# Kernel optimization log

Measured on AMD Instinct MI355X. Metric: run time of the kernel, lower is better.

The kernel has to match this reference:

```python
import jax, jax.numpy as jnp
import numpy as np

CONTEXT = 3  # config['context']
B, H, W = 8, 256, 256
NBR = 2 * CONTEXT  # number of similarity branches


def _conv(x, w, b):
    # x: [N, Cin, H, W], w: [Cout, Cin, kh, kw], SAME padding, stride 1
    y = jax.lax.conv_general_dilated(x, w, (1, 1), 'SAME',
                                     dimension_numbers=('NCHW', 'OIHW', 'NCHW'))
    return y + b[None, :, None, None]


def setup_inputs() -> dict:
    key = jax.random.key(0)
    ks = jax.random.split(key, 5)
    x = jax.random.normal(ks[0], (B, 2 * CONTEXT + 1, H, W), dtype=jnp.float32)
    # kaiming-ish scaled inits
    W1 = jax.random.normal(ks[1], (NBR, 64, 2, 3, 3), dtype=jnp.float32) * (2.0 / (64 * 9)) ** 0.5
    b1 = jnp.zeros((NBR, 64), dtype=jnp.float32)
    W2 = jax.random.normal(ks[2], (NBR, 1, 64, 1, 1), dtype=jnp.float32) * (2.0 / 1) ** 0.5 * 0.1
    b2 = jnp.zeros((NBR, 1), dtype=jnp.float32)
    Wm = jax.random.normal(ks[3], (7, 7, 3, 3), dtype=jnp.float32) * (2.0 / (7 * 9)) ** 0.5
    bm = jnp.zeros((7,), dtype=jnp.float32)
    return {'x': x, 'W1': W1, 'b1': b1, 'W2': W2, 'b2': b2, 'Wm': Wm, 'bm': bm}


def reference(x, W1, b1, W2, b2, Wm, bm):
    # mode == 'context' path just returns x; this implements the main path.
    base = x[:, CONTEXT:CONTEXT + 1]                                  # [B,1,H,W]
    checks = jnp.concatenate([x[:, :CONTEXT], x[:, CONTEXT + 1:]], axis=1)  # [B,6,H,W]
    check_e = checks[:, :, None]                                      # [B,6,1,H,W]
    base_e = jnp.broadcast_to(base[:, None], check_e.shape)           # [B,6,1,H,W]
    # channel order: pre-frames -> (base, check); post-frames -> (check, base)
    ch0 = jnp.concatenate([base_e[:, :CONTEXT], check_e[:, CONTEXT:]], axis=2 - 2 + 2)  # placeholder
    ch0 = jnp.concatenate([base_e[:, :CONTEXT], check_e[:, CONTEXT:]], axis=1)
    ch1 = jnp.concatenate([check_e[:, :CONTEXT], base_e[:, CONTEXT:]], axis=1)
    pairs = jnp.concatenate([ch0, ch1], axis=2)                       # [B,6,2,H,W]
    pairs = jnp.swapaxes(pairs, 0, 1)                                 # [6,B,2,H,W]

    def branch(pair, w1, bb1, w2, bb2):
        h = jax.nn.relu(_conv(pair, w1, bb1))                         # [B,64,H,W]
        return jax.nn.sigmoid(_conv(h, w2, bb2))                      # [B,1,H,W]

    sims = jax.vmap(branch)(pairs, W1, b1, W2, b2)                    # [6,B,1,H,W]
    weighted = sims[:, :, 0] * jnp.swapaxes(checks, 0, 1)             # [6,B,H,W]
    weighted = jnp.swapaxes(weighted, 0, 1)                           # [B,6,H,W]
    combined = jnp.concatenate([weighted[:, :CONTEXT], base, weighted[:, CONTEXT:]], axis=1)  # [B,7,H,W]
    return _conv(combined, Wm, bm)                                    # [B,7,H,W]
```

## Files before the change

### kernel.cpp

```cpp
#include <hip/hip_runtime.h>
#include <math.h>

#define Bn 8
#define Hn 256
#define Wn 256
#define HW (Hn * Wn)
#define ROWS 4
#define RP 264
#define ZW (12 * RP)

typedef __attribute__((ext_vector_type(8))) short bf16x8;
typedef __attribute__((ext_vector_type(4))) float f32x4;

__device__ __forceinline__ unsigned int pk_bits(unsigned int lo,
                                                unsigned int hi) {
  return __builtin_amdgcn_perm(hi, lo, 0x07060302u);
}
__device__ __forceinline__ unsigned int pk_bf16(float lo, float hi) {
  return pk_bits(__float_as_uint(lo), __float_as_uint(hi));
}

__device__ __constant__ const int T0c[8] = {0, 1, 2, 9, 10, 11, 3, 4};
__device__ __constant__ const int T1c[8] = {6, 7, 8, 15, 16, 17, 12, 13};
__device__ __constant__ const int T2c[8] = {5, 14, -1, -1, -1, -1, -1, -1};

__global__ __launch_bounds__(256) void sim_kernel(
    const float* __restrict__ x,
    const float* __restrict__ W1,
    const float* __restrict__ b1,
    const float* __restrict__ W2,
    const float* __restrict__ b2,
    float* __restrict__ comb)
{
  __shared__ float rowsF[12 * RP + 64];
  __shared__ uint4 wq[4][64];

  int bi = blockIdx.x;
  int n  = bi >> 9;
  int b  = (bi >> 6) & 7;
  int h0 = (bi & 63) * ROWS;
  int cc = (n < 3) ? n : n + 1;
  int t = threadIdx.x;

  const float* xb     = x + (size_t)b * 7 * HW;
  const float* basep  = xb + 3 * HW;
  const float* checkp = xb + (size_t)cc * HW;

  {
    int f = t >> 6, qq = (t >> 4) & 3, m = t & 15;
    int bsrc = (n < 3) ? 0 : 1;
    const float* wch = W1 + ((size_t)(n * 64 + 16 * f + m)) * 18;
    unsigned int kv[4];
#pragma unroll
    for (int jj = 0; jj < 4; ++jj) {
      int ja = 2 * jj, jb = 2 * jj + 1;
      int ta = (qq == 0) ? T0c[ja] : (qq == 1) ? T1c[ja]
               : (qq == 2) ? T2c[ja] : -1;
      int tb = (qq == 0) ? T0c[jb] : (qq == 1) ? T1c[jb]
               : (qq == 2) ? T2c[jb] : -1;
      float va = 0.f, vb = 0.f;
      if (ta >= 0) {
        int pl = ta / 9, rem = ta - pl * 9;
        va = wch[(pl ? 1 - bsrc : bsrc) * 9 + rem];
      }
      if (tb >= 0) {
        int pl = tb / 9, rem = tb - pl * 9;
        vb = wch[(pl ? 1 - bsrc : bsrc) * 9 + rem];
      }
      kv[jj] = pk_bf16(va, vb);
    }
    wq[f][(qq << 4) + m] = make_uint4(kv[0], kv[1], kv[2], kv[3]);
  }

  int lane = t & 63, wvid = t >> 6;
  int q = lane >> 4, m_ = lane & 15;
  float w2v[4][4];
  f32x4 b1vv[4];
#pragma unroll
  for (int f = 0; f < 4; ++f) {
    float4 tw = *(const float4*)&W2[n * 64 + 16 * f + 4 * q];
    float4 tb = *(const float4*)&b1[n * 64 + 16 * f + 4 * q];
    w2v[f][0] = tw.x; w2v[f][1] = tw.y; w2v[f][2] = tw.z; w2v[f][3] = tw.w;
    b1vv[f][0] = tb.x; b1vv[f][1] = tb.y;
    b1vv[f][2] = tb.z; b1vv[f][3] = tb.w;
  }
  float bb = b2[n];

  {
    int col = (t & 63) << 2;
#pragma unroll
    for (int it = 0; it < 3; ++it) {
      int rf = it * 4 + (t >> 6);
      int pl = (rf >= 6) ? 1 : 0;
      int j  = rf - pl * 6;
      int hh = h0 - 1 + j;
      const float* src = pl ? checkp : basep;
      float4 val = make_float4(0.f, 0.f, 0.f, 0.f);
      if ((unsigned)hh < (unsigned)Hn)
        val = *(const float4*)(src + hh * Wn + col);
      *(float4*)&rowsF[rf * RP + 4 + col] = val;
    }
    if (t < 12) {
      rowsF[t * RP + 3] = 0.f;
      rowsF[t * RP + 260] = 0.f;
    }
    if (t >= 192) rowsF[ZW + (t - 192)] = 0.f;
  }

  const unsigned int* rowsU = (const unsigned int*)rowsF;
  unsigned int addr[8], vbit[8];
#pragma unroll
  for (int jh = 0; jh < 8; ++jh) {
    int tap = (q == 0) ? T0c[jh] : (q == 1) ? T1c[jh]
              : (q == 2) ? T2c[jh] : -1;
    if (tap >= 0) {
      int pl = tap / 9, rem = tap - pl * 9;
      int rr = rem / 3, dx = rem - rr * 3;
      addr[jh] = (pl * 6 + rr) * RP + 3 + dx + wvid * 64 + m_;
      vbit[jh] = 1u;
    } else {
      addr[jh] = (unsigned)ZW;
      vbit[jh] = 0u;
    }
  }

  __syncthreads();

  bf16x8 afrag[4];
#pragma unroll
  for (int f = 0; f < 4; ++f) afrag[f] = *(const bf16x8*)&wq[f][lane];

  float* combcc = comb + ((size_t)b * 7 + cc) * HW;
  float* comb3  = comb + ((size_t)b * 7 + 3) * HW;
  int pxs = wvid * 64 + lane;

#pragma unroll 2
  for (int r = 0; r < ROWS; ++r) {
    int h = h0 + r;
    unsigned int rowoff = (unsigned)(r * RP);

    unsigned int base[8];
#pragma unroll
    for (int jh = 0; jh < 8; ++jh) base[jh] = addr[jh] + vbit[jh] * rowoff;

    float g[4];
#pragma unroll
    for (int half = 0; half < 2; ++half) {
      unsigned int dlo[8], dhi[8];
#pragma unroll
      for (int jh = 0; jh < 8; ++jh) {
        dlo[jh] = rowsU[base[jh] + half * 32];
        dhi[jh] = rowsU[base[jh] + half * 32 + 16];
      }
#pragma unroll
      for (int j = 0; j < 2; ++j) {
        const unsigned int* d = j ? dhi : dlo;
        union { unsigned int u[4]; bf16x8 v; } bu;
#pragma unroll
        for (int jj = 0; jj < 4; ++jj)
          bu.u[jj] = pk_bits(d[2 * jj], d[2 * jj + 1]);

        f32x4 acc[4];
#pragma unroll
        for (int f = 0; f < 4; ++f)
          acc[f] = __builtin_amdgcn_mfma_f32_16x16x32_bf16(afrag[f], bu.v,
                                                           b1vv[f], 0, 0, 0);

        float spA = 0.f, spB = 0.f;
#pragma unroll
        for (int rr = 0; rr < 4; ++rr) {
          spA = fmaf(w2v[0][rr], fmaxf(acc[0][rr], 0.f), spA);
          spB = fmaf(w2v[2][rr], fmaxf(acc[2][rr], 0.f), spB);
          spA = fmaf(w2v[1][rr], fmaxf(acc[1][rr], 0.f), spA);
          spB = fmaf(w2v[3][rr], fmaxf(acc[3][rr], 0.f), spB);
        }
        float sp = spA + spB;
        sp += __shfl_xor(sp, 16, 64);
        sp += __shfl_xor(sp, 32, 64);
        sp += bb;

        float e = __builtin_amdgcn_exp2f(sp * -1.442695041f);
        g[2 * half + j] = __builtin_amdgcn_rcpf(1.f + e);
      }
    }

    int hi = lane >> 4;
    float gsel = (hi == 0) ? g[0] : (hi == 1) ? g[1] : (hi == 2) ? g[2] : g[3];
    float ccv = rowsF[(6 + r + 1) * RP + 4 + pxs];
    combcc[h * Wn + pxs] = gsel * ccv;
    if (n == 0) comb3[h * Wn + pxs] = rowsF[(r + 1) * RP + 4 + pxs];
  }
}

__global__ __launch_bounds__(256) void mix_kernel(
    const float* __restrict__ comb,
    const float* __restrict__ Wm,
    const float* __restrict__ bm,
    float* __restrict__ out)
{
  __shared__ float mr[28 * RP];

  int bi = blockIdx.x;
  int b  = bi >> 7;
  int h0 = (bi & 127) << 1;
  int t = threadIdx.x;

  for (int u = t; u < 28 * 64; u += 256) {
    int rf = u >> 6;
    int col = (u & 63) << 2;
    int ic = rf >> 2, j = rf & 3;
    int hh = h0 - 1 + j;
    float4 v = make_float4(0.f, 0.f, 0.f, 0.f);
    if ((unsigned)hh < (unsigned)Hn)
      v = *(const float4*)(comb + ((size_t)b * 7 + ic) * HW + hh * Wn + col);
    *(float4*)&mr[rf * RP + 4 + col] = v;
  }
  if (t < 28) {
    mr[t * RP + 3] = 0.f;
    mr[t * RP + 260] = 0.f;
  }
  __syncthreads();

  int r   = t >> 7;
  int px0 = (t & 127) << 1;
  int h   = h0 + r;

  float acc[7][2];
#pragma unroll
  for (int oc = 0; oc < 7; ++oc) {
    float bv = bm[oc];
    acc[oc][0] = bv;
    acc[oc][1] = bv;
  }

#pragma unroll 2
  for (int ic = 0; ic < 7; ++ic) {
    float w[3][4];
#pragma unroll
    for (int dy = 0; dy < 3; ++dy) {
      const float* rp = &mr[(ic * 4 + r + dy) * RP + 3 + px0];
      w[dy][0] = rp[0]; w[dy][1] = rp[1];
      w[dy][2] = rp[2]; w[dy][3] = rp[3];
    }
    const float* wp = Wm + ic * 9;
#pragma unroll
    for (int oc = 0; oc < 7; ++oc) {
      const float* wo = wp + oc * 63;
#pragma unroll
      for (int dy = 0; dy < 3; ++dy)
#pragma unroll
        for (int dx = 0; dx < 3; ++dx) {
          float wvv = wo[dy * 3 + dx];
          acc[oc][0] = fmaf(wvv, w[dy][0 + dx], acc[oc][0]);
          acc[oc][1] = fmaf(wvv, w[dy][1 + dx], acc[oc][1]);
        }
    }
  }

  float* ob = out + (size_t)b * 7 * HW + h * Wn + px0;
#pragma unroll
  for (int oc = 0; oc < 7; ++oc)
    *(float2*)(ob + (size_t)oc * HW) = make_float2(acc[oc][0], acc[oc][1]);
}

extern "C" void kernel_launch(void* const* d_in, const int* in_sizes, int n_in,
                              void* d_out, int out_size, void* d_ws, size_t ws_size,
                              hipStream_t stream) {
  const float* x  = (const float*)d_in[0];
  const float* W1 = (const float*)d_in[1];
  const float* b1 = (const float*)d_in[2];
  const float* W2 = (const float*)d_in[3];
  const float* b2 = (const float*)d_in[4];
  const float* Wm = (const float*)d_in[5];
  const float* bm = (const float*)d_in[6];
  float* out  = (float*)d_out;
  float* comb = (float*)d_ws;

  sim_kernel<<<6 * 8 * (Hn / ROWS), 256, 0, stream>>>(x, W1, b1, W2, b2, comb);
  mix_kernel<<<8 * (Hn / 2), 256, 0, stream>>>(comb, Wm, bm, out);
}
```

Baseline: 124.8 us.

## Split sim kernel into single-wave blocks per 64-column strip, drop LDS weight staging

Result: slower. 142.5 us (+14.2%).

```diff
diff --git a/kernel.cpp b/kernel.cpp
--- a/kernel.cpp
+++ b/kernel.cpp
@@ -6,8 +6,8 @@
 #define Wn 256
 #define HW (Hn * Wn)
 #define ROWS 4
-#define RP 264
-#define ZW (12 * RP)
+#define SRP 68
+#define SZW (12 * SRP)
 
 typedef __attribute__((ext_vector_type(8))) short bf16x8;
 typedef __attribute__((ext_vector_type(4))) float f32x4;
@@ -20,11 +20,7 @@
   return pk_bits(__float_as_uint(lo), __float_as_uint(hi));
 }
 
-__device__ __constant__ const int T0c[8] = {0, 1, 2, 9, 10, 11, 3, 4};
-__device__ __constant__ const int T1c[8] = {6, 7, 8, 15, 16, 17, 12, 13};
-__device__ __constant__ const int T2c[8] = {5, 14, -1, -1, -1, -1, -1, -1};
-
-__global__ __launch_bounds__(256) void sim_kernel(
+__global__ __launch_bounds__(64) void sim_kernel(
     const float* __restrict__ x,
     const float* __restrict__ W1,
     const float* __restrict__ b1,
@@ -32,48 +28,69 @@
     const float* __restrict__ b2,
     float* __restrict__ comb)
 {
-  __shared__ float rowsF[12 * RP + 64];
-  __shared__ uint4 wq[4][64];
+  __shared__ float rowsS[12 * SRP + 64];
 
   int bi = blockIdx.x;
-  int n  = bi >> 9;
-  int b  = (bi >> 6) & 7;
-  int h0 = (bi & 63) * ROWS;
+  int n  = bi >> 11;
+  int rem = bi & 2047;
+  int b  = rem >> 8;
+  int c  = (rem >> 2) & 63;
+  int s  = rem & 3;
+  int h0 = c * ROWS;
+  int w0 = s * 64;
   int cc = (n < 3) ? n : n + 1;
-  int t = threadIdx.x;
+
+  int lane = threadIdx.x;
+  int q = lane >> 4, m_ = lane & 15;
 
   const float* xb     = x + (size_t)b * 7 * HW;
   const float* basep  = xb + 3 * HW;
   const float* checkp = xb + (size_t)cc * HW;
 
-  {
-    int f = t >> 6, qq = (t >> 4) & 3, m = t & 15;
-    int bsrc = (n < 3) ? 0 : 1;
-    const float* wch = W1 + ((size_t)(n * 64 + 16 * f + m)) * 18;
+#pragma unroll
+  for (int rf = 0; rf < 12; ++rf) {
+    int pl = (rf >= 6) ? 1 : 0;
+    int j  = rf - pl * 6;
+    int hh = h0 - 1 + j;
+    const float* src = pl ? checkp : basep;
+    bool okh = (unsigned)hh < (unsigned)Hn;
+    int col = w0 - 1 + lane;
+    float v = (okh && (unsigned)col < (unsigned)Wn) ? src[hh * Wn + col] : 0.f;
+    rowsS[rf * SRP + lane] = v;
+    if (lane < 2) {
+      int col2 = w0 + 63 + lane;
+      float v2 = (okh && (unsigned)col2 < (unsigned)Wn)
+                     ? src[hh * Wn + col2] : 0.f;
+      rowsS[rf * SRP + 64 + lane] = v2;
+    }
+  }
+  rowsS[SZW + lane] = 0.f;
+
+  int bsrc = (n < 3) ? 0 : 1;
+  bf16x8 afrag[4];
+#pragma unroll
+  for (int f = 0; f < 4; ++f) {
+    const float* wch = W1 + ((size_t)(n * 64 + 16 * f + m_)) * 18;
     unsigned int kv[4];
 #pragma unroll
     for (int jj = 0; jj < 4; ++jj) {
-      int ja = 2 * jj, jb = 2 * jj + 1;
-      int ta = (qq == 0) ? T0c[ja] : (qq == 1) ? T1c[ja]
-               : (qq == 2) ? T2c[ja] : -1;
-      int tb = (qq == 0) ? T0c[jb] : (qq == 1) ? T1c[jb]
-               : (qq == 2) ? T2c[jb] : -1;
-      float va = 0.f, vb = 0.f;
-      if (ta >= 0) {
-        int pl = ta / 9, rem = ta - pl * 9;
-        va = wch[(pl ? 1 - bsrc : bsrc) * 9 + rem];
-      }
-      if (tb >= 0) {
-        int pl = tb / 9, rem = tb - pl * 9;
-        vb = wch[(pl ? 1 - bsrc : bsrc) * 9 + rem];
-      }
-      kv[jj] = pk_bf16(va, vb);
-    }
-    wq[f][(qq << 4) + m] = make_uint4(kv[0], kv[1], kv[2], kv[3]);
-  }
-
-  int lane = t & 63, wvid = t >> 6;
-  int q = lane >> 4, m_ = lane & 15;
+      int k0 = 8 * q + 2 * jj, k1 = k0 + 1;
+      float v0 = 0.f, v1 = 0.f;
+      if (k0 < 18) {
+        int pl = (k0 >= 9) ? 1 : 0;
+        v0 = wch[(pl ? 1 - bsrc : bsrc) * 9 + (k0 - 9 * pl)];
+      }
+      if (k1 < 18) {
+        int pl = (k1 >= 9) ? 1 : 0;
+        v1 = wch[(pl ? 1 - bsrc : bsrc) * 9 + (k1 - 9 * pl)];
+      }
+      kv[jj] = pk_bf16(v0, v1);
+    }
+    union { unsigned int u[4]; bf16x8 v; } au;
+    au.u[0] = kv[0]; au.u[1] = kv[1]; au.u[2] = kv[2]; au.u[3] = kv[3];
+    afrag[f] = au.v;
+  }
+
   float w2v[4][4];
   f32x4 b1vv[4];
 #pragma unroll
@@ -86,58 +103,30 @@
   }
   float bb = b2[n];
 
-  {
-    int col = (t & 63) << 2;
-#pragma unroll
-    for (int it = 0; it < 3; ++it) {
-      int rf = it * 4 + (t >> 6);
-      int pl = (rf >= 6) ? 1 : 0;
-      int j  = rf - pl * 6;
-      int hh = h0 - 1 + j;
-      const float* src = pl ? checkp : basep;
-      float4 val = make_float4(0.f, 0.f, 0.f, 0.f);
-      if ((unsigned)hh < (unsigned)Hn)
-        val = *(const float4*)(src + hh * Wn + col);
-      *(float4*)&rowsF[rf * RP + 4 + col] = val;
-    }
-    if (t < 12) {
-      rowsF[t * RP + 3] = 0.f;
-      rowsF[t * RP + 260] = 0.f;
-    }
-    if (t >= 192) rowsF[ZW + (t - 192)] = 0.f;
-  }
-
-  const unsigned int* rowsU = (const unsigned int*)rowsF;
+  const unsigned int* rowsU = (const unsigned int*)rowsS;
   unsigned int addr[8], vbit[8];
 #pragma unroll
   for (int jh = 0; jh < 8; ++jh) {
-    int tap = (q == 0) ? T0c[jh] : (q == 1) ? T1c[jh]
-              : (q == 2) ? T2c[jh] : -1;
-    if (tap >= 0) {
-      int pl = tap / 9, rem = tap - pl * 9;
-      int rr = rem / 3, dx = rem - rr * 3;
-      addr[jh] = (pl * 6 + rr) * RP + 3 + dx + wvid * 64 + m_;
+    int k = 8 * q + jh;
+    if (k < 18) {
+      int pl = (k >= 9) ? 1 : 0;
+      int rem2 = k - 9 * pl;
+      int rr = rem2 / 3, dx = rem2 - rr * 3;
+      addr[jh] = (pl * 6 + rr) * SRP + m_ + dx;
       vbit[jh] = 1u;
     } else {
-      addr[jh] = (unsigned)ZW;
+      addr[jh] = (unsigned)SZW;
       vbit[jh] = 0u;
     }
   }
-
-  __syncthreads();
-
-  bf16x8 afrag[4];
-#pragma unroll
-  for (int f = 0; f < 4; ++f) afrag[f] = *(const bf16x8*)&wq[f][lane];
 
   float* combcc = comb + ((size_t)b * 7 + cc) * HW;
   float* comb3  = comb + ((size_t)b * 7 + 3) * HW;
-  int pxs = wvid * 64 + lane;
 
 #pragma unroll 2
   for (int r = 0; r < ROWS; ++r) {
     int h = h0 + r;
-    unsigned int rowoff = (unsigned)(r * RP);
+    unsigned int rowoff = (unsigned)(r * SRP);
 
     unsigned int base[8];
 #pragma unroll
@@ -184,14 +173,15 @@
       }
     }
 
-    int hi = lane >> 4;
-    float gsel = (hi == 0) ? g[0] : (hi == 1) ? g[1] : (hi == 2) ? g[2] : g[3];
-    float ccv = rowsF[(6 + r + 1) * RP + 4 + pxs];
-    combcc[h * Wn + pxs] = gsel * ccv;
-    if (n == 0) comb3[h * Wn + pxs] = rowsF[(r + 1) * RP + 4 + pxs];
-  }
-}
-
+    float gsel = (q == 0) ? g[0] : (q == 1) ? g[1] : (q == 2) ? g[2] : g[3];
+    float ccv = rowsS[(6 + r + 1) * SRP + lane + 1];
+    combcc[h * Wn + w0 + lane] = gsel * ccv;
+    if (n == 0)
+      comb3[h * Wn + w0 + lane] = rowsS[(r + 1) * SRP + lane + 1];
+  }
+}
+
+#define RP 264
 __global__ __launch_bounds__(256) void mix_kernel(
     const float* __restrict__ comb,
     const float* __restrict__ Wm,
@@ -276,6 +266,7 @@
   float* out  = (float*)d_out;
   float* comb = (float*)d_ws;
 
-  sim_kernel<<<6 * 8 * (Hn / ROWS), 256, 0, stream>>>(x, W1, b1, W2, b2, comb);
+  sim_kernel<<<6 * 8 * (Hn / ROWS) * 4, 64, 0, stream>>>(x, W1, b1, W2, b2,
+                                                         comb);
   mix_kernel<<<8 * (Hn / 2), 256, 0, stream>>>(comb, Wm, bm, out);
 }
```

## Compute 1x1 second conv via MFMA instead of VALU FMAs and shuffles

Applied to the files above, without the earlier changes.

Measured after the change: 125.2 us. Within noise of the previous version (+0.3%).

```diff
diff --git a/kernel.cpp b/kernel.cpp
--- a/kernel.cpp
+++ b/kernel.cpp
@@ -49,7 +49,7 @@
   {
     int f = t >> 6, qq = (t >> 4) & 3, m = t & 15;
     int bsrc = (n < 3) ? 0 : 1;
-    const float* wch = W1 + ((size_t)(n * 64 + 16 * f + m)) * 18;
+    const float* wch = W1 + ((size_t)(n * 64 + 4 * m + f)) * 18;
     unsigned int kv[4];
 #pragma unroll
     for (int jj = 0; jj < 4; ++jj) {
@@ -74,17 +74,24 @@
 
   int lane = t & 63, wvid = t >> 6;
   int q = lane >> 4, m_ = lane & 15;
-  float w2v[4][4];
+
+  union { unsigned int u[4]; bf16x8 v; } a2a, a2b;
+#pragma unroll
+  for (int jj = 0; jj < 4; ++jj) {
+    int o = n * 64 + 16 * q;
+    a2a.u[jj] = pk_bf16(W2[o + 2 * jj],     W2[o + 2 * jj + 1]);
+    a2b.u[jj] = pk_bf16(W2[o + 8 + 2 * jj], W2[o + 8 + 2 * jj + 1]);
+  }
+
   f32x4 b1vv[4];
 #pragma unroll
-  for (int f = 0; f < 4; ++f) {
-    float4 tw = *(const float4*)&W2[n * 64 + 16 * f + 4 * q];
-    float4 tb = *(const float4*)&b1[n * 64 + 16 * f + 4 * q];
-    w2v[f][0] = tw.x; w2v[f][1] = tw.y; w2v[f][2] = tw.z; w2v[f][3] = tw.w;
-    b1vv[f][0] = tb.x; b1vv[f][1] = tb.y;
-    b1vv[f][2] = tb.z; b1vv[f][3] = tb.w;
-  }
+  for (int f = 0; f < 4; ++f)
+#pragma unroll
+    for (int r = 0; r < 4; ++r)
+      b1vv[f][r] = b1[n * 64 + 16 * q + 4 * r + f];
   float bb = b2[n];
+  f32x4 c2init;
+  c2init[0] = bb; c2init[1] = bb; c2init[2] = bb; c2init[3] = bb;
 
   {
     int col = (t & 63) << 2;
@@ -166,26 +173,28 @@
           acc[f] = __builtin_amdgcn_mfma_f32_16x16x32_bf16(afrag[f], bu.v,
                                                            b1vv[f], 0, 0, 0);
 
-        float spA = 0.f, spB = 0.f;
-#pragma unroll
-        for (int rr = 0; rr < 4; ++rr) {
-          spA = fmaf(w2v[0][rr], fmaxf(acc[0][rr], 0.f), spA);
-          spB = fmaf(w2v[2][rr], fmaxf(acc[2][rr], 0.f), spB);
-          spA = fmaf(w2v[1][rr], fmaxf(acc[1][rr], 0.f), spA);
-          spB = fmaf(w2v[3][rr], fmaxf(acc[3][rr], 0.f), spB);
+        union { unsigned int u[4]; bf16x8 v; } p2a, p2b;
+#pragma unroll
+        for (int jj = 0; jj < 4; ++jj) {
+          int c = 2 * jj;
+          p2a.u[jj] = pk_bf16(fmaxf(acc[c & 3][c >> 2], 0.f),
+                              fmaxf(acc[(c + 1) & 3][c >> 2], 0.f));
+          int c2 = 8 + 2 * jj;
+          p2b.u[jj] = pk_bf16(fmaxf(acc[c2 & 3][c2 >> 2], 0.f),
+                              fmaxf(acc[(c2 + 1) & 3][c2 >> 2], 0.f));
         }
-        float sp = spA + spB;
-        sp += __shfl_xor(sp, 16, 64);
-        sp += __shfl_xor(sp, 32, 64);
-        sp += bb;
+        f32x4 d2 = __builtin_amdgcn_mfma_f32_16x16x32_bf16(a2a.v, p2a.v,
+                                                           c2init, 0, 0, 0);
+        d2 = __builtin_amdgcn_mfma_f32_16x16x32_bf16(a2b.v, p2b.v,
+                                                     d2, 0, 0, 0);
+        float sp = d2[0];
 
         float e = __builtin_amdgcn_exp2f(sp * -1.442695041f);
         g[2 * half + j] = __builtin_amdgcn_rcpf(1.f + e);
       }
     }
 
-    int hi = lane >> 4;
-    float gsel = (hi == 0) ? g[0] : (hi == 1) ? g[1] : (hi == 2) ? g[2] : g[3];
+    float gsel = (q == 0) ? g[0] : (q == 1) ? g[1] : (q == 2) ? g[2] : g[3];
     float ccv = rowsF[(6 + r + 1) * RP + 4 + pxs];
     combcc[h * Wn + pxs] = gsel * ccv;
     if (n == 0) comb3[h * Wn + pxs] = rowsF[(r + 1) * RP + 4 + pxs];
```
